# Optimization experiments

Measured on AMD Instinct MI355X. Metric: run time of the kernel, lower is better.

The kernel has to match this reference:

```python
import jax, jax.numpy as jnp
import numpy as np

N, INT_DIM = 4096, 512
X_DIMS = [128, 128, 128, 128]
DIM_LIST = list(zip(X_DIMS[:-1], X_DIMS[1:]))
TOT_DIM = sum(d0 * d1 + d1 for d0, d1 in DIM_LIST)  # 49536
FUNS = [jax.nn.relu, jax.nn.relu, None]


def setup_inputs() -> dict:
    key = jax.random.key(0)
    k1, k2, k3, k4 = jax.random.split(key, 4)
    int_x = jax.random.normal(k1, (N, INT_DIM), dtype=jnp.float32)
    x = jax.random.normal(k2, (N, X_DIMS[0]), dtype=jnp.float32)
    # torch Linear(IntDim, tot_dim): W [out, in], b [out]; scale like kaiming-uniform-ish
    W = jax.random.normal(k3, (TOT_DIM, INT_DIM), dtype=jnp.float32) * (1.0 / np.sqrt(INT_DIM))
    b = jax.random.normal(k4, (TOT_DIM,), dtype=jnp.float32) * 0.02
    return {"int_x": int_x, "x": x, "W": W, "b": b}


def reference(int_x, x, W, b):
    # hypernetwork: per-sample generated weights/biases, [N, tot_dim]
    temp = jnp.einsum('ni,oi->no', int_x, W) + b
    cum = 0
    h = x
    for (d0, d1), fun in zip(DIM_LIST, FUNS):
        bias = temp[:, cum:cum + d1]                                   # [N, d1]
        weight = temp[:, cum + d1:cum + d1 + d0 * d1].reshape(-1, d0, d1)  # [N, d0, d1]
        cum += d1 + d0 * d1
        h = jnp.einsum('npq,np->nq', weight, h) + bias
        if fun is not None:
            h = fun(h)
    return h
```

## Files before the change

### kernel.cpp

```cpp
#include <hip/hip_runtime.h>
#include <cstdint>
#include <cstddef>

#define NSAMP 4096
#define KDIM  512
#define TOT   49536
#define NUMN  387
#define BK    64
#define LCHUNK 16512

typedef __attribute__((ext_vector_type(8))) __bf16 bf16x8;
typedef __attribute__((ext_vector_type(4))) __bf16 bf16x4;
typedef __attribute__((ext_vector_type(4))) float  f32x4;

#define AS1 __attribute__((address_space(1)))
#define AS3 __attribute__((address_space(3)))

__global__ void cast_bf16(const float* __restrict__ in, __bf16* __restrict__ out, int n4) {
    int i = blockIdx.x * blockDim.x + threadIdx.x;
    int stride = gridDim.x * blockDim.x;
    for (; i < n4; i += stride) {
        float4 v = ((const float4*)in)[i];
        bf16x4 o = { (__bf16)v.x, (__bf16)v.y, (__bf16)v.z, (__bf16)v.w };
        ((bf16x4*)out)[i] = o;
    }
}

__global__ __launch_bounds__(256) void hyper_gemm(
    const __bf16* __restrict__ A, const __bf16* __restrict__ B,
    const float* __restrict__ bias, __bf16* __restrict__ C)
{
    __shared__ __bf16 As[128 * BK];
    __shared__ __bf16 Bs[128 * BK];

    const int tid   = threadIdx.x;
    const int lane  = tid & 63;
    const int quad  = lane >> 4;
    const int r16   = lane & 15;
    const int wv    = tid >> 6;
    const int waveM = wv >> 1;
    const int waveN = wv & 1;

    const int num_m = gridDim.y;
    const int id    = blockIdx.y * NUMN + blockIdx.x;
    const int gsz   = 8 * num_m;
    const int s     = id / gsz;
    const int r     = id % gsz;
    const int base  = s * 8;
    int w = NUMN - base; if (w > 8) w = 8;
    const int n_t = base + r % w;
    const int m_t = r / w;

    const int m0 = m_t * 128;
    const int n0 = n_t * 128;

    f32x4 acc[4][4] = {};

    const __bf16* gAp[4];
    const __bf16* gBp[4];
    int ldsOff[4];
#pragma unroll
    for (int c = 0; c < 4; ++c) {
        int idx  = c * 256 + tid;
        int row  = idx >> 3;
        int gsrc = (idx & 7) ^ (row & 7);
        gAp[c] = A + (size_t)(m0 + row) * KDIM + gsrc * 8;
        gBp[c] = B + (size_t)(n0 + row) * KDIM + gsrc * 8;
        ldsOff[c] = idx * 8;
    }

    const int rsw = r16 & 7;

    for (int kt = 0; kt < KDIM / BK; ++kt) {
        const int k0 = kt * BK;
#pragma unroll
        for (int c = 0; c < 4; ++c) {
            __builtin_amdgcn_global_load_lds((AS1 void*)(gAp[c] + k0),
                (AS3 void*)(As + ldsOff[c]), 16, 0, 0);
            __builtin_amdgcn_global_load_lds((AS1 void*)(gBp[c] + k0),
                (AS3 void*)(Bs + ldsOff[c]), 16, 0, 0);
        }
        __syncthreads();

#pragma unroll
        for (int kk = 0; kk < 2; ++kk) {
            bf16x8 af[4], bf[4];
#pragma unroll
            for (int i = 0; i < 4; ++i) {
                int rr = waveM * 64 + i * 16 + r16;
                af[i] = *(const bf16x8*)(As + rr * BK + (((kk * 4 + quad) ^ rsw) * 8));
            }
#pragma unroll
            for (int j = 0; j < 4; ++j) {
                int rr = waveN * 64 + j * 16 + r16;
                bf[j] = *(const bf16x8*)(Bs + rr * BK + (((kk * 4 + quad) ^ rsw) * 8));
            }
#pragma unroll
            for (int i = 0; i < 4; ++i)
#pragma unroll
                for (int j = 0; j < 4; ++j)
                    acc[i][j] = __builtin_amdgcn_mfma_f32_16x16x32_bf16(af[i], bf[j], acc[i][j], 0, 0, 0);
        }
        __syncthreads();
    }

#pragma unroll
    for (int j = 0; j < 4; ++j) {
        int n = n0 + waveN * 64 + j * 16 + r16;
        float bb = bias[n];
#pragma unroll
        for (int i = 0; i < 4; ++i) {
            int mbase = m0 + waveM * 64 + i * 16 + quad * 4;
#pragma unroll
            for (int rr = 0; rr < 4; ++rr) {
                C[(size_t)(mbase + rr) * TOT + n] = (__bf16)(acc[i][j][rr] + bb);
            }
        }
    }
}

__global__ __launch_bounds__(256) void mlp_kernel(
    const float* __restrict__ x, const __bf16* __restrict__ temp,
    float* __restrict__ out, int samp0)
{
    const int n   = samp0 + blockIdx.x;
    const int tid = threadIdx.x;
    const int wv  = tid >> 6;
    const int l   = tid & 63;
    const int pg  = l >> 4;
    const int qg  = l & 15;

    __shared__ float h[128];
    __shared__ float partial[4][128];

    if (tid < 64) ((float2*)h)[tid] = ((const float2*)(x + (size_t)n * 128))[tid];

    const __bf16* row = temp + (size_t)blockIdx.x * TOT;

    bf16x8 w[8];
#pragma unroll
    for (int i = 0; i < 8; ++i)
        w[i] = *(const bf16x8*)(row + 128 + (size_t)(wv * 32 + i * 4 + pg) * 128 + qg * 8);

    int cum = 0;
#pragma unroll
    for (int layer = 0; layer < 3; ++layer) {
        bf16x8 wn[8];
        if (layer < 2) {
#pragma unroll
            for (int i = 0; i < 8; ++i)
                wn[i] = *(const bf16x8*)(row + cum + LCHUNK + 128
                        + (size_t)(wv * 32 + i * 4 + pg) * 128 + qg * 8);
        }
        float bv = 0.f;
        if (tid < 128) bv = (float)row[cum + tid];

        float acc[8] = {0, 0, 0, 0, 0, 0, 0, 0};
        __syncthreads();
#pragma unroll
        for (int i = 0; i < 8; ++i) {
            float hp = h[wv * 32 + i * 4 + pg];
#pragma unroll
            for (int j = 0; j < 8; ++j) acc[j] += (float)w[i][j] * hp;
        }
#pragma unroll
        for (int j = 0; j < 8; ++j) {
            acc[j] += __shfl_xor(acc[j], 16);
            acc[j] += __shfl_xor(acc[j], 32);
        }
        if (pg == 0) {
#pragma unroll
            for (int j = 0; j < 8; ++j) partial[wv][qg * 8 + j] = acc[j];
        }
        __syncthreads();
        if (tid < 128) {
            float v = partial[0][tid] + partial[1][tid] + partial[2][tid] + partial[3][tid]
                    + bv;
            if (layer < 2) v = fmaxf(v, 0.f);
            h[tid] = v;
        }
        if (layer < 2) {
#pragma unroll
            for (int i = 0; i < 8; ++i) w[i] = wn[i];
        }
        cum += LCHUNK;
    }
    __syncthreads();
    if (tid < 64) ((float2*)(out + (size_t)n * 128))[tid] = ((const float2*)h)[tid];
}

extern "C" void kernel_launch(void* const* d_in, const int* in_sizes, int n_in,
                              void* d_out, int out_size, void* d_ws, size_t ws_size,
                              hipStream_t stream) {
    const float* int_x = (const float*)d_in[0];
    const float* x     = (const float*)d_in[1];
    const float* W     = (const float*)d_in[2];
    const float* b     = (const float*)d_in[3];
    float* out = (float*)d_out;

    char* ws = (char*)d_ws;
    __bf16* A_bf = (__bf16*)ws;
    size_t offA = (size_t)NSAMP * KDIM * 2;
    __bf16* W_bf = (__bf16*)(ws + offA);
    size_t offW = offA + (size_t)TOT * KDIM * 2;
    __bf16* temp = (__bf16*)(ws + offW);

    size_t remain = (ws_size > offW) ? (ws_size - offW) : 0;
    int chunk = 128;
    for (int c = 4096; c >= 128; c >>= 1) {
        if ((size_t)c * TOT * 2 <= remain) { chunk = c; break; }
    }

    int nA4 = NSAMP * KDIM / 4;
    cast_bf16<<<(nA4 + 255) / 256, 256, 0, stream>>>(int_x, A_bf, nA4);
    int nW4 = TOT * KDIM / 4;
    cast_bf16<<<(nW4 + 255) / 256, 256, 0, stream>>>(W, W_bf, nW4);

    for (int samp0 = 0; samp0 < NSAMP; samp0 += chunk) {
        dim3 grid(NUMN, chunk / 128);
        hyper_gemm<<<grid, 256, 0, stream>>>(A_bf + (size_t)samp0 * KDIM, W_bf, b, temp);
        mlp_kernel<<<chunk, 256, 0, stream>>>(x, temp, out, samp0);
    }
}
```

Measured before the change: 534.2 us.

## Rewrite hypernetwork GEMM with 256x256 tiles and ping-pong double-buffered LDS

Replaces the 128x128 single-buffered GEMM with a 512-thread kernel computing 256x256 output tiles. It double-buffers A and B in 128KB of LDS and issues async global-to-LDS loads in a hand-interleaved schedule using explicit waitcnt, barriers and setprio around MFMA bursts. The output column count is padded to a multiple of 256, so temp rows use a padded stride and the MLP kernel reads with it. The aim is more operand reuse per loaded byte and hiding load latency behind MFMA work. In exchange, LDS use limits each CU to one block, and the padded B rows read uninitialized workspace whose results land in unused columns.

```diff
diff --git a/kernel.cpp b/kernel.cpp
--- a/kernel.cpp
+++ b/kernel.cpp
@@ -5,8 +5,8 @@
 #define NSAMP 4096
 #define KDIM  512
 #define TOT   49536
-#define NUMN  387
-#define BK    64
+#define TOT_P 49664
+#define NUMN_P 194
 #define LCHUNK 16512
 
 typedef __attribute__((ext_vector_type(8))) __bf16 bf16x8;
@@ -26,97 +26,157 @@
     }
 }
 
-__global__ __launch_bounds__(256) void hyper_gemm(
+__global__ __launch_bounds__(512, 2) void hyper_gemm(
     const __bf16* __restrict__ A, const __bf16* __restrict__ B,
     const float* __restrict__ bias, __bf16* __restrict__ C)
 {
-    __shared__ __bf16 As[128 * BK];
-    __shared__ __bf16 Bs[128 * BK];
-
-    const int tid   = threadIdx.x;
-    const int lane  = tid & 63;
-    const int quad  = lane >> 4;
-    const int r16   = lane & 15;
-    const int wv    = tid >> 6;
-    const int waveM = wv >> 1;
-    const int waveN = wv & 1;
+    __shared__ __bf16 lds[65536];
+    __bf16* Ae = lds;
+    __bf16* Be = lds + 16384;
+    __bf16* Ao = lds + 32768;
+    __bf16* Bo = lds + 49152;
+
+    const int tid  = threadIdx.x;
+    const int lane = tid & 63;
+    const int quad = lane >> 4;
+    const int r16  = lane & 15;
+    const int wv   = tid >> 6;
+    const int waveN = wv & 3;
+    const int waveM = wv >> 2;
 
     const int num_m = gridDim.y;
-    const int id    = blockIdx.y * NUMN + blockIdx.x;
-    const int gsz   = 8 * num_m;
-    const int s     = id / gsz;
-    const int r     = id % gsz;
-    const int base  = s * 8;
-    int w = NUMN - base; if (w > 8) w = 8;
+    const int id  = blockIdx.y * gridDim.x + blockIdx.x;
+    const int gsz = 8 * num_m;
+    const int sg  = id / gsz;
+    const int r   = id % gsz;
+    const int base = sg * 8;
+    int w = gridDim.x - base; if (w > 8) w = 8;
     const int n_t = base + r % w;
     const int m_t = r / w;
-
-    const int m0 = m_t * 128;
-    const int n0 = n_t * 128;
-
-    f32x4 acc[4][4] = {};
-
-    const __bf16* gAp[4];
-    const __bf16* gBp[4];
-    int ldsOff[4];
-#pragma unroll
-    for (int c = 0; c < 4; ++c) {
-        int idx  = c * 256 + tid;
-        int row  = idx >> 3;
-        int gsrc = (idx & 7) ^ (row & 7);
-        gAp[c] = A + (size_t)(m0 + row) * KDIM + gsrc * 8;
-        gBp[c] = B + (size_t)(n0 + row) * KDIM + gsrc * 8;
-        ldsOff[c] = idx * 8;
-    }
+    const int m0 = m_t * 256;
+    const int n0 = n_t * 256;
+
+    const int row0 = tid >> 3;
+    const int g0   = tid & 7;
+    const int aO0 = (m0 + row0) * KDIM + ((g0 ^ (row0 & 7)) * 8);
+    const int aO1 = aO0 + 64 * KDIM;
+    const int bO0 = (n0 + row0) * KDIM + ((g0 ^ (row0 & 7)) * 8);
+    const int bO1 = bO0 + 64 * KDIM;
+    const int ldsO0 = tid * 8;
+    const int ldsO1 = 4096 + tid * 8;
+
+#define STAGE_A(REG, half, tile) do { \
+    __builtin_amdgcn_global_load_lds((AS1 void*)(A + aO0 + (half)*65536 + (tile)*64), \
+        (AS3 void*)((REG) + (half)*8192 + ldsO0), 16, 0, 0); \
+    __builtin_amdgcn_global_load_lds((AS1 void*)(A + aO1 + (half)*65536 + (tile)*64), \
+        (AS3 void*)((REG) + (half)*8192 + ldsO1), 16, 0, 0); \
+} while (0)
+#define STAGE_B(REG, half, tile) do { \
+    __builtin_amdgcn_global_load_lds((AS1 void*)(B + bO0 + (half)*65536 + (tile)*64), \
+        (AS3 void*)((REG) + (half)*8192 + ldsO0), 16, 0, 0); \
+    __builtin_amdgcn_global_load_lds((AS1 void*)(B + bO1 + (half)*65536 + (tile)*64), \
+        (AS3 void*)((REG) + (half)*8192 + ldsO1), 16, 0, 0); \
+} while (0)
 
     const int rsw = r16 & 7;
-
-    for (int kt = 0; kt < KDIM / BK; ++kt) {
-        const int k0 = kt * BK;
-#pragma unroll
-        for (int c = 0; c < 4; ++c) {
-            __builtin_amdgcn_global_load_lds((AS1 void*)(gAp[c] + k0),
-                (AS3 void*)(As + ldsOff[c]), 16, 0, 0);
-            __builtin_amdgcn_global_load_lds((AS1 void*)(gBp[c] + k0),
-                (AS3 void*)(Bs + ldsOff[c]), 16, 0, 0);
-        }
-        __syncthreads();
-
-#pragma unroll
-        for (int kk = 0; kk < 2; ++kk) {
-            bf16x8 af[4], bf[4];
-#pragma unroll
-            for (int i = 0; i < 4; ++i) {
-                int rr = waveM * 64 + i * 16 + r16;
-                af[i] = *(const bf16x8*)(As + rr * BK + (((kk * 4 + quad) ^ rsw) * 8));
-            }
-#pragma unroll
-            for (int j = 0; j < 4; ++j) {
-                int rr = waveN * 64 + j * 16 + r16;
-                bf[j] = *(const bf16x8*)(Bs + rr * BK + (((kk * 4 + quad) ^ rsw) * 8));
-            }
-#pragma unroll
-            for (int i = 0; i < 4; ++i)
-#pragma unroll
-                for (int j = 0; j < 4; ++j)
-                    acc[i][j] = __builtin_amdgcn_mfma_f32_16x16x32_bf16(af[i], bf[j], acc[i][j], 0, 0, 0);
-        }
-        __syncthreads();
-    }
+    const int aRd = (waveM * 128 + r16) * 64;
+    const int bRd = (waveN * 64 + r16) * 64;
+    const int kg0 = ((0 * 4 + quad) ^ rsw) * 8;
+    const int kg1 = ((1 * 4 + quad) ^ rsw) * 8;
+
+    f32x4 acc[8][4] = {};
+    bf16x8 af[4][2], bf0[2][2], bf1[2][2];
+
+#define LDA_(BUF, mq) { _Pragma("unroll") for (int i4 = 0; i4 < 4; ++i4) { \
+    af[i4][0] = *(const bf16x8*)((BUF) + aRd + (mq)*4096 + i4*1024 + kg0); \
+    af[i4][1] = *(const bf16x8*)((BUF) + aRd + (mq)*4096 + i4*1024 + kg1); } }
+#define LDB0_(BUF) { _Pragma("unroll") for (int j2 = 0; j2 < 2; ++j2) { \
+    bf0[j2][0] = *(const bf16x8*)((BUF) + bRd + j2*1024 + kg0); \
+    bf0[j2][1] = *(const bf16x8*)((BUF) + bRd + j2*1024 + kg1); } }
+#define LDB1_(BUF) { _Pragma("unroll") for (int j2 = 0; j2 < 2; ++j2) { \
+    bf1[j2][0] = *(const bf16x8*)((BUF) + bRd + 2048 + j2*1024 + kg0); \
+    bf1[j2][1] = *(const bf16x8*)((BUF) + bRd + 2048 + j2*1024 + kg1); } }
+#define MFMA16_(MQ, NQ, BF) { _Pragma("unroll") for (int i4 = 0; i4 < 4; ++i4) \
+    _Pragma("unroll") for (int j2 = 0; j2 < 2; ++j2) { \
+      acc[(MQ)*4+i4][(NQ)*2+j2] = __builtin_amdgcn_mfma_f32_16x16x32_bf16( \
+          af[i4][0], BF[j2][0], acc[(MQ)*4+i4][(NQ)*2+j2], 0, 0, 0); \
+      acc[(MQ)*4+i4][(NQ)*2+j2] = __builtin_amdgcn_mfma_f32_16x16x32_bf16( \
+          af[i4][1], BF[j2][1], acc[(MQ)*4+i4][(NQ)*2+j2], 0, 0, 0); } }
+
+#define BARRIER_ asm volatile("s_barrier" ::: "memory")
+#define LGKM8_   asm volatile("s_waitcnt lgkmcnt(8)" ::: "memory")
+#define LGKM0_   asm volatile("s_waitcnt lgkmcnt(0)" ::: "memory"); __builtin_amdgcn_sched_barrier(0)
+#define PRIO1_   __builtin_amdgcn_s_setprio(1)
+#define PRIO0_   __builtin_amdgcn_s_setprio(0); __builtin_amdgcn_sched_barrier(0)
+#define VM4_     asm volatile("s_waitcnt vmcnt(4)" ::: "memory")
+#define VM0_     asm volatile("s_waitcnt vmcnt(0)" ::: "memory")
+
+    STAGE_B(Be, 0, 0); STAGE_B(Be, 1, 0);
+    STAGE_A(Ae, 0, 0); STAGE_A(Ae, 1, 0);
+    STAGE_B(Bo, 0, 1); STAGE_B(Bo, 1, 1);
+    VM4_; BARRIER_;
+
+    for (int it = 0; it < 3; ++it) {
+        const int t = 2 * it;
+        LDA_(Ae, 0); LDB0_(Be); STAGE_A(Ao, 0, t + 1); LGKM8_;
+        BARRIER_; LGKM0_; PRIO1_; MFMA16_(0, 0, bf0); PRIO0_; BARRIER_;
+        LDB1_(Be); STAGE_A(Ao, 1, t + 1);
+        BARRIER_; LGKM0_; PRIO1_; MFMA16_(0, 1, bf1); PRIO0_; BARRIER_;
+        LDA_(Ae, 1); STAGE_B(Be, 0, t + 2);
+        BARRIER_; LGKM0_; PRIO1_; MFMA16_(1, 0, bf0); PRIO0_; BARRIER_;
+        STAGE_B(Be, 1, t + 2);
+        BARRIER_; LGKM0_; PRIO1_; MFMA16_(1, 1, bf1); PRIO0_; VM4_; BARRIER_;
+        LDA_(Ao, 0); LDB0_(Bo); STAGE_A(Ae, 0, t + 2); LGKM8_;
+        BARRIER_; LGKM0_; PRIO1_; MFMA16_(0, 0, bf0); PRIO0_; BARRIER_;
+        LDB1_(Bo); STAGE_A(Ae, 1, t + 2);
+        BARRIER_; LGKM0_; PRIO1_; MFMA16_(0, 1, bf1); PRIO0_; BARRIER_;
+        LDA_(Ao, 1); STAGE_B(Bo, 0, t + 3);
+        BARRIER_; LGKM0_; PRIO1_; MFMA16_(1, 0, bf0); PRIO0_; BARRIER_;
+        STAGE_B(Bo, 1, t + 3);
+        BARRIER_; LGKM0_; PRIO1_; MFMA16_(1, 1, bf1); PRIO0_; VM4_; BARRIER_;
+    }
+
+    LDA_(Ae, 0); LDB0_(Be); STAGE_A(Ao, 0, 7); LGKM8_;
+    BARRIER_; LGKM0_; PRIO1_; MFMA16_(0, 0, bf0); PRIO0_; BARRIER_;
+    LDB1_(Be); STAGE_A(Ao, 1, 7);
+    BARRIER_; LGKM0_; PRIO1_; MFMA16_(0, 1, bf1); PRIO0_; BARRIER_;
+    LDA_(Ae, 1);
+    BARRIER_; LGKM0_; PRIO1_; MFMA16_(1, 0, bf0); PRIO0_; BARRIER_;
+    BARRIER_; LGKM0_; PRIO1_; MFMA16_(1, 1, bf1); PRIO0_; VM0_; BARRIER_;
+    LDA_(Ao, 0); LDB0_(Bo);
+    BARRIER_; LGKM0_; PRIO1_; MFMA16_(0, 0, bf0); PRIO0_; BARRIER_;
+    LDB1_(Bo);
+    BARRIER_; LGKM0_; PRIO1_; MFMA16_(0, 1, bf1); PRIO0_; BARRIER_;
+    LDA_(Ao, 1);
+    BARRIER_; LGKM0_; PRIO1_; MFMA16_(1, 0, bf0); PRIO0_; BARRIER_;
+    BARRIER_; LGKM0_; PRIO1_; MFMA16_(1, 1, bf1); PRIO0_;
 
 #pragma unroll
     for (int j = 0; j < 4; ++j) {
         int n = n0 + waveN * 64 + j * 16 + r16;
-        float bb = bias[n];
-#pragma unroll
-        for (int i = 0; i < 4; ++i) {
-            int mbase = m0 + waveM * 64 + i * 16 + quad * 4;
+        float bb = (n < TOT) ? bias[n] : 0.f;
+#pragma unroll
+        for (int i = 0; i < 8; ++i) {
+            int mrow = m0 + waveM * 128 + i * 16 + quad * 4;
 #pragma unroll
             for (int rr = 0; rr < 4; ++rr) {
-                C[(size_t)(mbase + rr) * TOT + n] = (__bf16)(acc[i][j][rr] + bb);
+                C[(size_t)(mrow + rr) * TOT_P + n] = (__bf16)(acc[i][j][rr] + bb);
             }
         }
     }
+#undef STAGE_A
+#undef STAGE_B
+#undef LDA_
+#undef LDB0_
+#undef LDB1_
+#undef MFMA16_
+#undef BARRIER_
+#undef LGKM8_
+#undef LGKM0_
+#undef PRIO1_
+#undef PRIO0_
+#undef VM4_
+#undef VM0_
 }
 
 __global__ __launch_bounds__(256) void mlp_kernel(
@@ -135,7 +195,7 @@
 
     if (tid < 64) ((float2*)h)[tid] = ((const float2*)(x + (size_t)n * 128))[tid];
 
-    const __bf16* row = temp + (size_t)blockIdx.x * TOT;
+    const __bf16* row = temp + (size_t)blockIdx.x * TOT_P;
 
     bf16x8 w[8];
 #pragma unroll
@@ -202,13 +262,13 @@
     __bf16* A_bf = (__bf16*)ws;
     size_t offA = (size_t)NSAMP * KDIM * 2;
     __bf16* W_bf = (__bf16*)(ws + offA);
-    size_t offW = offA + (size_t)TOT * KDIM * 2;
+    size_t offW = offA + (size_t)TOT_P * KDIM * 2;
     __bf16* temp = (__bf16*)(ws + offW);
 
     size_t remain = (ws_size > offW) ? (ws_size - offW) : 0;
-    int chunk = 128;
-    for (int c = 4096; c >= 128; c >>= 1) {
-        if ((size_t)c * TOT * 2 <= remain) { chunk = c; break; }
+    int chunk = 256;
+    for (int c = 4096; c >= 256; c >>= 1) {
+        if ((size_t)c * TOT_P * 2 <= remain) { chunk = c; break; }
     }
 
     int nA4 = NSAMP * KDIM / 4;
@@ -217,8 +277,8 @@
     cast_bf16<<<(nW4 + 255) / 256, 256, 0, stream>>>(W, W_bf, nW4);
 
     for (int samp0 = 0; samp0 < NSAMP; samp0 += chunk) {
-        dim3 grid(NUMN, chunk / 128);
-        hyper_gemm<<<grid, 256, 0, stream>>>(A_bf + (size_t)samp0 * KDIM, W_bf, b, temp);
+        dim3 grid(NUMN_P, chunk / 256);
+        hyper_gemm<<<grid, 512, 0, stream>>>(A_bf + (size_t)samp0 * KDIM, W_bf, b, temp);
         mlp_kernel<<<chunk, 256, 0, stream>>>(x, temp, out, samp0);
     }
 }
```

New measurement: 531.6 us. No clear change (-0.5%).

## Double-buffer LDS tiles in hyper_gemm to overlap global loads with MFMA

Applied to the files above, without the earlier changes.

The GEMM now keeps two LDS buffers for the A and B tiles. While the MFMAs run on the current K-tile, it issues the async global-to-LDS loads for the next one, so there is one barrier per iteration instead of a load, wait, compute sequence. It also adds a launch bound hint of 2 blocks per CU. The cost is double the LDS use (64KB per block), which can lower occupancy, and more register pressure from the hint.

```diff
diff --git a/kernel.cpp b/kernel.cpp
--- a/kernel.cpp
+++ b/kernel.cpp
@@ -26,12 +26,12 @@
     }
 }
 
-__global__ __launch_bounds__(256) void hyper_gemm(
+__global__ __launch_bounds__(256, 2) void hyper_gemm(
     const __bf16* __restrict__ A, const __bf16* __restrict__ B,
     const float* __restrict__ bias, __bf16* __restrict__ C)
 {
-    __shared__ __bf16 As[128 * BK];
-    __shared__ __bf16 Bs[128 * BK];
+    __shared__ __bf16 As[2][128 * BK];
+    __shared__ __bf16 Bs[2][128 * BK];
 
     const int tid   = threadIdx.x;
     const int lane  = tid & 63;
@@ -69,18 +69,28 @@
         ldsOff[c] = idx * 8;
     }
 
+#define STAGE(buf, k0) do { \
+    _Pragma("unroll") \
+    for (int c = 0; c < 4; ++c) { \
+        __builtin_amdgcn_global_load_lds((AS1 void*)(gAp[c] + (k0)), \
+            (AS3 void*)(&As[buf][0] + ldsOff[c]), 16, 0, 0); \
+        __builtin_amdgcn_global_load_lds((AS1 void*)(gBp[c] + (k0)), \
+            (AS3 void*)(&Bs[buf][0] + ldsOff[c]), 16, 0, 0); \
+    } \
+} while (0)
+
     const int rsw = r16 & 7;
 
+    STAGE(0, 0);
+    __syncthreads();
+
     for (int kt = 0; kt < KDIM / BK; ++kt) {
-        const int k0 = kt * BK;
-#pragma unroll
-        for (int c = 0; c < 4; ++c) {
-            __builtin_amdgcn_global_load_lds((AS1 void*)(gAp[c] + k0),
-                (AS3 void*)(As + ldsOff[c]), 16, 0, 0);
-            __builtin_amdgcn_global_load_lds((AS1 void*)(gBp[c] + k0),
-                (AS3 void*)(Bs + ldsOff[c]), 16, 0, 0);
-        }
-        __syncthreads();
+        const int cur = kt & 1;
+        if (kt < KDIM / BK - 1) {
+            STAGE(cur ^ 1, (kt + 1) * BK);
+        }
+        const __bf16* Ab = &As[cur][0];
+        const __bf16* Bb = &Bs[cur][0];
 
 #pragma unroll
         for (int kk = 0; kk < 2; ++kk) {
@@ -88,12 +98,12 @@
 #pragma unroll
             for (int i = 0; i < 4; ++i) {
                 int rr = waveM * 64 + i * 16 + r16;
-                af[i] = *(const bf16x8*)(As + rr * BK + (((kk * 4 + quad) ^ rsw) * 8));
+                af[i] = *(const bf16x8*)(Ab + rr * BK + (((kk * 4 + quad) ^ rsw) * 8));
             }
 #pragma unroll
             for (int j = 0; j < 4; ++j) {
                 int rr = waveN * 64 + j * 16 + r16;
-                bf[j] = *(const bf16x8*)(Bs + rr * BK + (((kk * 4 + quad) ^ rsw) * 8));
+                bf[j] = *(const bf16x8*)(Bb + rr * BK + (((kk * 4 + quad) ^ rsw) * 8));
             }
 #pragma unroll
             for (int i = 0; i < 4; ++i)
@@ -117,6 +127,7 @@
             }
         }
     }
+#undef STAGE
 }
 
 __global__ __launch_bounds__(256) void mlp_kernel(
```

After: 540.7 us. About the same (+1.2%).

## Stage full-K A tile in LDS and stream B from global into registers

Applied to the files above, without the earlier changes.

The GEMM now loads the block's entire 128x512 A tile into LDS once, with an XOR swizzle, before the main loop. B fragments are read straight from global memory into registers, double-buffered one K-step ahead, which removes the per-iteration LDS staging of B and the barriers inside the loop. The cost is 128KB of LDS per block, so launch bounds are set to one block per CU and occupancy drops. The A load is also no longer overlapped with compute, and the two M-waves issue duplicate global loads for the same B rows.

```diff
diff --git a/kernel.cpp b/kernel.cpp
--- a/kernel.cpp
+++ b/kernel.cpp
@@ -6,7 +6,6 @@
 #define KDIM  512
 #define TOT   49536
 #define NUMN  387
-#define BK    64
 #define LCHUNK 16512
 
 typedef __attribute__((ext_vector_type(8))) __bf16 bf16x8;
@@ -26,12 +25,11 @@
     }
 }
 
-__global__ __launch_bounds__(256) void hyper_gemm(
+__global__ __launch_bounds__(256, 1) void hyper_gemm(
     const __bf16* __restrict__ A, const __bf16* __restrict__ B,
     const float* __restrict__ bias, __bf16* __restrict__ C)
 {
-    __shared__ __bf16 As[128 * BK];
-    __shared__ __bf16 Bs[128 * BK];
+    __shared__ __bf16 As[128 * KDIM];
 
     const int tid   = threadIdx.x;
     const int lane  = tid & 63;
@@ -56,64 +54,67 @@
 
     f32x4 acc[4][4] = {};
 
-    const __bf16* gAp[4];
-    const __bf16* gBp[4];
-    int ldsOff[4];
-#pragma unroll
-    for (int c = 0; c < 4; ++c) {
-        int idx  = c * 256 + tid;
-        int row  = idx >> 3;
-        int gsrc = (idx & 7) ^ (row & 7);
-        gAp[c] = A + (size_t)(m0 + row) * KDIM + gsrc * 8;
-        gBp[c] = B + (size_t)(n0 + row) * KDIM + gsrc * 8;
-        ldsOff[c] = idx * 8;
-    }
+    {
+        const __bf16* aE = A + (size_t)(m0 + wv) * KDIM
+                         + (lane >> 3) * 64 + ((lane & 7) ^ wv) * 8;
+        const __bf16* aO = A + (size_t)(m0 + wv) * KDIM
+                         + (lane >> 3) * 64 + (((lane & 7) ^ wv) ^ 4) * 8;
+#pragma unroll
+        for (int p = 0; p < 32; ++p) {
+            const __bf16* src = ((p & 1) ? aO : aE) + (size_t)p * 4 * KDIM;
+            __builtin_amdgcn_global_load_lds((AS1 void*)src,
+                (AS3 void*)(As + ((p * 256 + tid) * 8)), 16, 0, 0);
+        }
+    }
+
+    const __bf16* gB = B + (size_t)(n0 + waveN * 64 + r16) * KDIM + quad * 8;
+
+    bf16x8 bb[2][4][2];
+#define LOADB(par, kt) { _Pragma("unroll") for (int j = 0; j < 4; ++j) { \
+    _Pragma("unroll") for (int kk = 0; kk < 2; ++kk) { \
+        bb[par][j][kk] = *(const bf16x8*)(gB + (size_t)j * 16 * KDIM + (kt) * 64 + kk * 32); } } }
 
     const int rsw = r16 & 7;
 
-    for (int kt = 0; kt < KDIM / BK; ++kt) {
-        const int k0 = kt * BK;
-#pragma unroll
-        for (int c = 0; c < 4; ++c) {
-            __builtin_amdgcn_global_load_lds((AS1 void*)(gAp[c] + k0),
-                (AS3 void*)(As + ldsOff[c]), 16, 0, 0);
-            __builtin_amdgcn_global_load_lds((AS1 void*)(gBp[c] + k0),
-                (AS3 void*)(Bs + ldsOff[c]), 16, 0, 0);
-        }
-        __syncthreads();
-
-#pragma unroll
-        for (int kk = 0; kk < 2; ++kk) {
-            bf16x8 af[4], bf[4];
-#pragma unroll
-            for (int i = 0; i < 4; ++i) {
-                int rr = waveM * 64 + i * 16 + r16;
-                af[i] = *(const bf16x8*)(As + rr * BK + (((kk * 4 + quad) ^ rsw) * 8));
+    LOADB(0, 0);
+    __syncthreads();
+
+#pragma unroll
+    for (int kt = 0; kt < 8; ++kt) {
+        const int cur = kt & 1;
+        if (kt < 7) LOADB(cur ^ 1, kt + 1);
+
+        bf16x8 af[4][2];
+#pragma unroll
+        for (int i = 0; i < 4; ++i) {
+            int rr = waveM * 64 + i * 16 + r16;
+#pragma unroll
+            for (int kk = 0; kk < 2; ++kk)
+                af[i][kk] = *(const bf16x8*)(As + rr * KDIM + kt * 64
+                                             + (((kk * 4 + quad) ^ rsw) * 8));
+        }
+#pragma unroll
+        for (int i = 0; i < 4; ++i)
+#pragma unroll
+            for (int j = 0; j < 4; ++j) {
+                acc[i][j] = __builtin_amdgcn_mfma_f32_16x16x32_bf16(
+                    af[i][0], bb[cur][j][0], acc[i][j], 0, 0, 0);
+                acc[i][j] = __builtin_amdgcn_mfma_f32_16x16x32_bf16(
+                    af[i][1], bb[cur][j][1], acc[i][j], 0, 0, 0);
             }
-#pragma unroll
-            for (int j = 0; j < 4; ++j) {
-                int rr = waveN * 64 + j * 16 + r16;
-                bf[j] = *(const bf16x8*)(Bs + rr * BK + (((kk * 4 + quad) ^ rsw) * 8));
-            }
-#pragma unroll
-            for (int i = 0; i < 4; ++i)
-#pragma unroll
-                for (int j = 0; j < 4; ++j)
-                    acc[i][j] = __builtin_amdgcn_mfma_f32_16x16x32_bf16(af[i], bf[j], acc[i][j], 0, 0, 0);
-        }
-        __syncthreads();
-    }
+    }
+#undef LOADB
 
 #pragma unroll
     for (int j = 0; j < 4; ++j) {
         int n = n0 + waveN * 64 + j * 16 + r16;
-        float bb = bias[n];
+        float bb2 = bias[n];
 #pragma unroll
         for (int i = 0; i < 4; ++i) {
             int mbase = m0 + waveM * 64 + i * 16 + quad * 4;
 #pragma unroll
             for (int rr = 0; rr < 4; ++rr) {
-                C[(size_t)(mbase + rr) * TOT + n] = (__bf16)(acc[i][j][rr] + bb);
+                C[(size_t)(mbase + rr) * TOT + n] = (__bf16)(acc[i][j][rr] + bb2);
             }
         }
     }
```

After: 751.6 us. 40.7% more time.
